# Performance work log

Hardware: AMD Instinct MI355X
Metric: run time of the kernel (lower is better)

Reference implementation:

```python
import jax, jax.numpy as jnp
import numpy as np

S = 1024        # img_size
RADIUS = 512    # number of radial bins
WEIGHT = 1.0


def _bin_idx():
    # Matches torch.meshgrid(arange(-s/2, s/2), ..., indexing='ij') with +0.5 offsets.
    xs = jnp.arange(-S / 2, S / 2, dtype=jnp.float32)
    d = jnp.sqrt((xs[:, None] + 0.5) ** 2 + (xs[None, :] + 0.5) ** 2)  # [S, S]
    # Bin edges are integers 0..RADIUS, so mask (d>=r)&(d<r+1) == (floor(d)==r).
    idx = jnp.floor(d).astype(jnp.int32)
    # Pixels with d >= RADIUS fall in no mask -> overflow bucket RADIUS (dropped later).
    return jnp.where(d < RADIUS, idx, RADIUS).reshape(-1)  # [S*S]


def _power_spec(image):
    ft = jnp.fft.fft2(image)                 # [B, C, S, S] complex
    return jnp.fft.fftshift(jnp.abs(ft) ** 2, axes=(-2, -1))


def _radial_power_spec(ps2d, idx):
    B, C = ps2d.shape[0], ps2d.shape[1]
    flat = ps2d.reshape(B * C, S * S)
    # Histogram reduction: O(S*S) instead of the original O(RADIUS*S*S) dense mask multiply.
    seg = jax.vmap(lambda v: jax.ops.segment_sum(v, idx, num_segments=RADIUS + 1))(flat)
    rad = seg[:, :RADIUS] / (S * S)          # mean over (H, W), drop overflow bucket
    return rad.reshape(B, C, RADIUS).sum(axis=1)  # sum over channel dim


def setup_inputs() -> dict:
    key = jax.random.key(0)
    k1, k2 = jax.random.split(key)
    output = jax.random.normal(k1, (16, 1, S, S), dtype=jnp.float32)
    target = jax.random.normal(k2, (16, 1, S, S), dtype=jnp.float32)
    return {"output": output, "target": target}


def reference(output, target):
    idx = _bin_idx()
    ps_out = _radial_power_spec(_power_spec(output), idx)   # [B, RADIUS]
    ps_tgt = _radial_power_spec(_power_spec(target), idx)   # [B, RADIUS]
    return jnp.mean(jnp.abs(ps_out - ps_tgt)) * WEIGHT
```

## Files before the change

kernel.cpp:

```cpp
#include <hip/hip_runtime.h>
#include <math.h>

#define S 1024
#define RADIUS 512
#define NIMG 32
#define PBX 129

__device__ __forceinline__ float2 cmul(float2 a, float2 b) {
    return make_float2(a.x * b.x - a.y * b.y, a.x * b.y + a.y * b.x);
}
__device__ __forceinline__ float2 cadd(float2 a, float2 b) { return make_float2(a.x + b.x, a.y + b.y); }
__device__ __forceinline__ float2 csub(float2 a, float2 b) { return make_float2(a.x - b.x, a.y - b.y); }

__device__ const float2 C16[8] = {
    {1.0f, 0.0f},
    {0.92387953251128674f, -0.38268343236508978f},
    {0.70710678118654757f, -0.70710678118654746f},
    {0.38268343236508984f, -0.92387953251128674f},
    {0.0f, -1.0f},
    {-0.38268343236508973f, -0.92387953251128674f},
    {-0.70710678118654746f, -0.70710678118654757f},
    {-0.92387953251128663f, -0.38268343236508989f},
};
__device__ const float2 C8T[4] = {
    {1.0f, 0.0f},
    {0.70710678118654757f, -0.70710678118654746f},
    {0.0f, -1.0f},
    {-0.70710678118654746f, -0.70710678118654757f},
};
__device__ const float2 W512T[8] = {
    {1.0f, 0.0f},
    {0.99992470183914454f, -0.012271538285719925f},
    {0.99969881869620425f, -0.024541228522912288f},
    {0.99932238458834954f, -0.036807222941358832f},
    {0.99879545620517241f, -0.049067674327418015f},
    {0.99811811290014918f, -0.061320736302208578f},
    {0.99729045667869021f, -0.073564563599667426f},
    {0.99631261218277800f, -0.085797312344439894f},
};
__device__ const float2 W64T[8] = {
    {1.0f, 0.0f},
    {0.99518472667219693f, -0.098017140329560604f},
    {0.98078528040323044f, -0.19509032201612825f},
    {0.95694033573220886f, -0.29028467725446233f},
    {0.92387953251128674f, -0.38268343236508978f},
    {0.88192126434835505f, -0.47139673682599764f},
    {0.83146961230254524f, -0.55557023301960218f},
    {0.77301045336273699f, -0.63439328416364549f},
};
__device__ const float2 W128P[8] = {
    {1.0f, 0.0f},
    {0.99879545620517241f, -0.049067674327418015f},
    {0.99518472667219693f, -0.098017140329560604f},
    {0.98917650996478101f, -0.14673047445536175f},
    {0.98078528040323044f, -0.19509032201612825f},
    {0.97003125319454397f, -0.24298017990326390f},
    {0.95694033573220886f, -0.29028467725446233f},
    {0.94154406518302081f, -0.33688985339222005f},
};
__device__ const float2 W1024P[8] = {
    {1.0f, 0.0f},
    {0.99998117528260111f, -0.0061358846491544753f},
    {0.99992470183914454f, -0.012271538285719925f},
    {0.99983058179582340f, -0.018406729905804820f},
    {0.99969881869620425f, -0.024541228522912288f},
    {0.99952941750109314f, -0.030674803176636626f},
    {0.99932238458834954f, -0.036807222941358832f},
    {0.99907772775264536f, -0.042938256934940820f},
};

__device__ __forceinline__ void fft16(float2 r[16], float2 T) {
    float2 tc[8];
    #pragma unroll
    for (int u = 0; u < 8; ++u) tc[u] = cmul(T, C16[u]);
    #pragma unroll
    for (int u = 0; u < 8; ++u) {
        float2 a = r[u], b = r[u + 8];
        r[u] = cadd(a, b);
        r[u + 8] = cmul(csub(a, b), tc[u]);
    }
    T = cmul(T, T);
    #pragma unroll
    for (int u = 0; u < 4; ++u) tc[u] = cmul(T, C16[2 * u]);
    #pragma unroll
    for (int g = 0; g < 2; ++g)
        #pragma unroll
        for (int u = 0; u < 4; ++u) {
            int lo = g * 8 + u;
            float2 a = r[lo], b = r[lo + 4];
            r[lo] = cadd(a, b);
            r[lo + 4] = cmul(csub(a, b), tc[u]);
        }
    T = cmul(T, T);
    #pragma unroll
    for (int u = 0; u < 2; ++u) tc[u] = cmul(T, C16[4 * u]);
    #pragma unroll
    for (int g = 0; g < 4; ++g)
        #pragma unroll
        for (int u = 0; u < 2; ++u) {
            int lo = g * 4 + u;
            float2 a = r[lo], b = r[lo + 2];
            r[lo] = cadd(a, b);
            r[lo + 2] = cmul(csub(a, b), tc[u]);
        }
    T = cmul(T, T);
    #pragma unroll
    for (int g = 0; g < 8; ++g) {
        int lo = g * 2;
        float2 a = r[lo], b = r[lo + 1];
        r[lo] = cadd(a, b);
        r[lo + 1] = cmul(csub(a, b), T);
    }
}

__device__ __forceinline__ void fft8(float2 r[8], float2 T) {
    float2 tc[4];
    #pragma unroll
    for (int u = 0; u < 4; ++u) tc[u] = cmul(T, C8T[u]);
    #pragma unroll
    for (int u = 0; u < 4; ++u) {
        float2 a = r[u], b = r[u + 4];
        r[u] = cadd(a, b);
        r[u + 4] = cmul(csub(a, b), tc[u]);
    }
    T = cmul(T, T);
    #pragma unroll
    for (int u = 0; u < 2; ++u) tc[u] = cmul(T, C8T[2 * u]);
    #pragma unroll
    for (int g = 0; g < 2; ++g)
        #pragma unroll
        for (int u = 0; u < 2; ++u) {
            int lo = g * 4 + u;
            float2 a = r[lo], b = r[lo + 2];
            r[lo] = cadd(a, b);
            r[lo + 2] = cmul(csub(a, b), tc[u]);
        }
    T = cmul(T, T);
    #pragma unroll
    for (int g = 0; g < 4; ++g) {
        int lo = g * 2;
        float2 a = r[lo], b = r[lo + 1];
        r[lo] = cadd(a, b);
        r[lo + 1] = cmul(csub(a, b), T);
    }
}

__device__ __forceinline__ void fft_last2(float2 r[16], int c) {
    #pragma unroll
    for (int m = 0; m < 16; ++m) {
        float vx = __shfl_xor(r[m].x, 2, 64);
        float vy = __shfl_xor(r[m].y, 2, 64);
        if (c & 2) {
            float dx = vx - r[m].x, dy = vy - r[m].y;
            if (c & 1) { r[m].x = dy; r[m].y = -dx; }
            else       { r[m].x = dx; r[m].y = dy; }
        } else {
            r[m].x += vx; r[m].y += vy;
        }
    }
    #pragma unroll
    for (int m = 0; m < 16; ++m) {
        float vx = __shfl_xor(r[m].x, 1, 64);
        float vy = __shfl_xor(r[m].y, 1, 64);
        if (c & 1) { r[m].x = vx - r[m].x; r[m].y = vy - r[m].y; }
        else       { r[m].x += vx; r[m].y += vy; }
    }
}

__device__ __forceinline__ int bitrev3(int x) {
    return ((x & 1) << 2) | (x & 2) | ((x >> 2) & 1);
}

__global__ __launch_bounds__(512, 4)
void fft_rows(const float* __restrict__ outp, const float* __restrict__ tgtp,
              float2* __restrict__ WpT, int imgBase) {
    __shared__ float2 buf[4096];
    const int t = threadIdx.x;
    const int w = t >> 6, tau = t & 63;
    const int yy = blockIdx.x * 8 + w;
    const int i = blockIdx.y, g = imgBase + i;
    const float* img = (g < 16 ? outp : tgtp) + (size_t)(g & 15) * S * S;
    const float* r0 = img + (size_t)(2 * yy) * S;
    const float* r1 = r0 + S;

    float2 r[16];
    #pragma unroll
    for (int j = 0; j < 16; ++j) r[j] = make_float2(r0[64 * j + tau], r1[64 * j + tau]);

    fft16(r, cmul(W128P[tau >> 3], W1024P[tau & 7]));

    float2* wb = buf + (w << 9);
    const int b = tau >> 2, c = tau & 3;
    float2 ex[8];
    #pragma unroll
    for (int j = 0; j < 8; ++j) wb[(j << 6) | (tau ^ (j << 2))] = r[j];
    if (b < 8) {
        #pragma unroll
        for (int m = 0; m < 8; ++m)  r[m]      = wb[((b & 7) << 6) + 4 * ((m ^ b) & 15) + c];
        #pragma unroll
        for (int m = 8; m < 16; ++m) ex[m - 8] = wb[((b & 7) << 6) + 4 * ((m ^ b) & 15) + c];
    }
    #pragma unroll
    for (int j = 8; j < 16; ++j) wb[((j & 7) << 6) | (tau ^ (j << 2))] = r[j];
    if (b >= 8) {
        #pragma unroll
        for (int m = 0; m < 8; ++m)  r[m]      = wb[((b & 7) << 6) + 4 * ((m ^ b) & 15) + c];
        #pragma unroll
        for (int m = 8; m < 16; ++m) ex[m - 8] = wb[((b & 7) << 6) + 4 * ((m ^ b) & 15) + c];
    }
    #pragma unroll
    for (int m = 8; m < 16; ++m) r[m] = ex[m - 8];

    fft16(r, W64T[c]);
    fft_last2(r, c);

    const int yy0 = blockIdx.x * 8;
    float2* dst = WpT + (size_t)i * 512 * 1024;
    #pragma unroll
    for (int h = 0; h < 2; ++h) {
        if ((c & 1) == h) {
            #pragma unroll
            for (int m = 0; m < 16; ++m) {
                int n = (b << 6) + 4 * m + c;
                int kh = (int)(__brev((unsigned)n) >> 22) & 511;
                buf[(w << 9) | (kh ^ (w << 1))] = r[m];
            }
        }
        __syncthreads();
        #pragma unroll
        for (int q = 0; q < 8; ++q) {
            int idx = q * 512 + t;
            int uu = idx >> 3, wv = idx & 7;
            float2 val = buf[(wv << 9) | (uu ^ (wv << 1))];
            dst[(size_t)(uu + (h << 9)) * 512 + yy0 + wv] = val;
        }
        __syncthreads();
    }
}

__global__ __launch_bounds__(512, 4)
void fft_cols_bin2(const float2* __restrict__ WpT, float* __restrict__ partial, int imgBase) {
    __shared__ float2 tbuf[8 * 512];
    __shared__ float pref[512];
    __shared__ float cws[8];
    __shared__ float cwx[8];
    const int t = threadIdx.x;
    const int w = t >> 6, tau = t & 63;
    const int i = blockIdx.y, g = imgBase + i;
    const int l = w >> 1;
    const int u = blockIdx.x * 4 + l;
    const int setb = w & 1;
    const bool active = (u <= 512);

    const int b3 = tau >> 3, lam = tau & 7;
    float2 X[8];
    float2* mb = tbuf + (w << 9);

    if (active) {
        const float2* Wimg = WpT + (size_t)i * 512 * 1024;
        const int mu = (1024 - u) & 1023;
        const float2* rowA = Wimg + (size_t)u * 512;
        const float2* rowM = Wimg + (size_t)mu * 512;

        #pragma unroll
        for (int j = 0; j < 8; ++j) {
            float2 A = rowA[64 * j + tau];
            float2 M = rowM[64 * j + tau];
            X[j] = (setb == 0)
                 ? make_float2(0.5f * (A.x + M.x), 0.5f * (A.y - M.y))
                 : make_float2(0.5f * (A.y + M.y), 0.5f * (M.x - A.x));
        }

        fft8(X, cmul(W64T[b3], W512T[lam]));

        #pragma unroll
        for (int j = 0; j < 8; ++j) mb[(j << 6) | (tau ^ (j << 3) ^ j)] = X[j];
        #pragma unroll
        for (int c = 0; c < 8; ++c) X[c] = mb[(b3 << 6) | (((c ^ b3) << 3) | (lam ^ b3))];

        fft8(X, W64T[lam]);

        #pragma unroll
        for (int c = 0; c < 8; ++c) mb[(b3 << 6) | (((c ^ b3) << 3) | (lam ^ b3))] = X[c];
        #pragma unroll
        for (int d = 0; d < 8; ++d) X[d] = mb[(b3 << 6) | (((lam ^ b3) << 3) | (d ^ b3))];

        fft8(X, make_float2(1.0f, 0.0f));

        const int base9 = 8 * bitrev3(lam) + bitrev3(b3);
        #pragma unroll
        for (int d = 0; d < 8; ++d) {
            mb[(bitrev3(d) << 6) + base9] = X[d];
        }
    }
    __syncthreads();

    float p[8];
    if (active) {
        const float2* b0 = tbuf + ((w & ~1) << 9);
        const float2* b1 = tbuf + ((w | 1) << 9);
        const float2 Wtau = cmul(W128P[tau >> 3], W1024P[tau & 7]);
        #pragma unroll
        for (int m = 0; m < 8; ++m) {
            const int f = tau + 64 * m;
            float2 x0 = b0[f];
            float2 x1 = b1[f];
            float2 Wf = cmul(Wtau, C16[m]);
            float2 wx = cmul(Wf, x1);
            float2 G = (setb == 0) ? cadd(x0, wx)
                                   : csub(x0, wx);
            p[m] = G.x * G.x + G.y * G.y;
        }
    }
    __syncthreads();

    float* Prow = (float*)tbuf;
    if (active) {
        #pragma unroll
        for (int m = 0; m < 8; ++m) {
            const int v = tau + 64 * m + (setb << 9);
            Prow[(l << 10) + v] = p[m];
        }
    }
    __syncthreads();

    const int r = t;
    const float r2  = (float)(r * r);
    const float r12 = (float)((r + 1) * (r + 1));
    float acc = 0.0f;

    for (int rowi = 0; rowi < 8; ++rowi) {
        const int ll = rowi >> 1;
        const int mir = rowi & 1;
        const int uu = blockIdx.x * 4 + ll;
        const bool valid = (uu <= 512) && (!mir || (uu >= 1 && uu <= 511));
        float F = 0.0f;
        if (valid) {
            const float* PR = Prow + (ll << 10);
            F = mir ? (PR[t + 1] + PR[(1024 - t) & 1023])
                    : (PR[t] + PR[1023 - t]);
        }
        float s = F;
        #pragma unroll
        for (int off = 1; off < 64; off <<= 1) {
            float n = __shfl_up(s, off, 64);
            if (tau >= off) s += n;
        }
        pref[t] = s;
        if (tau == 63) cws[w] = s;
        __syncthreads();
        if (t < 8) {
            float x = 0.0f;
            #pragma unroll
            for (int j = 0; j < 8; ++j) {
                if (j < t) x += cws[j];
            }
            cwx[t] = x;
        }
        __syncthreads();
        if (valid) {
            const float cuv = mir ? ((float)uu - 0.5f)
                                  : ((uu < 512) ? ((float)uu + 0.5f) : 511.5f);
            const float cu2 = cuv * cuv;
            const float Bv = r12 - cu2;
            if (Bv > 0.0f) {
                const float Av = r2 - cu2;
                float cvlo = (Av > 0.0f) ? sqrtf(Av) : 0.0f;
                float cvhi = sqrtf(Bv);
                int vlo = (int)ceilf(cvlo - 0.5f);
                int vhi = (int)ceilf(cvhi - 0.5f);
                if (vhi > 512) vhi = 512;
                if (vlo < 0) vlo = 0;
                if (vhi > vlo) {
                    float hi = pref[vhi - 1] + cwx[(vhi - 1) >> 6];
                    float lo = (vlo > 0) ? (pref[vlo - 1] + cwx[(vlo - 1) >> 6]) : 0.0f;
                    acc += hi - lo;
                }
            }
        }
        __syncthreads();
    }
    partial[(((size_t)g * PBX) + blockIdx.x) * 512 + t] = acc;
}

__global__ __launch_bounds__(512)
void reduce_partials(const float* __restrict__ partial, float* __restrict__ rad) {
    const int g = blockIdx.x;
    const int t = threadIdx.x;
    const float* p = partial + (size_t)g * PBX * 512;
    float s = 0.0f;
    for (int b = 0; b < PBX; ++b) s += p[(size_t)b * 512 + t];
    rad[(size_t)g * 512 + t] = s;
}

__global__ __launch_bounds__(256)
void final_loss(const float* __restrict__ rad, float* __restrict__ out) {
    __shared__ float red[256];
    const int t = threadIdx.x;
    float acc = 0.0f;
    for (int i = t; i < 16 * RADIUS; i += 256) {
        int bb = i >> 9;
        int rr = i & (RADIUS - 1);
        float o = rad[(size_t)bb * RADIUS + rr];
        float gg = rad[(size_t)(bb + 16) * RADIUS + rr];
        acc += fabsf(o - gg);
    }
    red[t] = acc;
    __syncthreads();
    for (int off = 128; off > 0; off >>= 1) {
        if (t < off) red[t] += red[t + off];
        __syncthreads();
    }
    if (t == 0) {
        out[0] = red[0] / ((float)S * (float)S) / (16.0f * (float)RADIUS);
    }
}

extern "C" void kernel_launch(void* const* d_in, const int* in_sizes, int n_in,
                              void* d_out, int out_size, void* d_ws, size_t ws_size,
                              hipStream_t stream) {
    const float* outp = (const float*)d_in[0];
    const float* tgtp = (const float*)d_in[1];
    float* dout = (float*)d_out;

    char* ws = (char*)d_ws;
    float* rad = (float*)ws;
    const size_t partBytes = (size_t)NIMG * PBX * 512 * sizeof(float);
    float* partial = (float*)(ws + 65536);
    float2* WpT = (float2*)(ws + 65536 + partBytes);
    const size_t perImg = (size_t)512 * 1024 * sizeof(float2);
    size_t used = 65536 + partBytes;
    size_t avail = (ws_size > used) ? (ws_size - used) : 0;
    int chunk = (int)(avail / perImg);
    if (chunk > NIMG) chunk = NIMG;
    if (chunk < 1) chunk = 1;

    for (int base = 0; base < NIMG; base += chunk) {
        int c = (NIMG - base < chunk) ? (NIMG - base) : chunk;
        fft_rows<<<dim3(64, c), 512, 0, stream>>>(outp, tgtp, WpT, base);
        fft_cols_bin2<<<dim3(PBX, c), 512, 0, stream>>>(WpT, partial, base);
    }

    reduce_partials<<<NIMG, 512, 0, stream>>>(partial, rad);
    final_loss<<<1, 256, 0, stream>>>(rad, dout);
}
```

Before: 174.9 us.

## Vectorize row loads/stores and make radial binning wave-local without block barriers

The row FFT now loads input rows with float4 reads staged through shared memory and writes the transposed output with float4 stores instead of scalar float2 accesses. In the column/binning kernel, each wave now owns one (row, mirror) pair and computes its full 512-entry prefix sum with a shuffle carry, so the per-row block-wide barriers and cross-wave scan fixup go away. Each wave then evaluates all 512 radii for its row, and the per-wave bin results are summed across waves through shared memory. This removes many __syncthreads calls at the cost of more per-thread registers (acc[8]) and extra shared-memory traffic.

New measurement: 163.9 us. 1.07x faster.

```diff
diff --git a/kernel.cpp b/kernel.cpp
--- a/kernel.cpp
+++ b/kernel.cpp
@@ -183,13 +183,27 @@
     const float* r0 = img + (size_t)(2 * yy) * S;
     const float* r1 = r0 + S;
 
+    float2* wb = buf + (w << 9);
+    float* wf = (float*)wb;
+
     float2 r[16];
     #pragma unroll
-    for (int j = 0; j < 16; ++j) r[j] = make_float2(r0[64 * j + tau], r1[64 * j + tau]);
+    for (int q = 0; q < 4; ++q) {
+        float4 v = *reinterpret_cast<const float4*>(&r0[q * 256 + 4 * tau]);
+        *reinterpret_cast<float4*>(&wf[q * 256 + 4 * tau]) = v;
+    }
+    #pragma unroll
+    for (int j = 0; j < 16; ++j) r[j].x = wf[64 * j + tau];
+    #pragma unroll
+    for (int q = 0; q < 4; ++q) {
+        float4 v = *reinterpret_cast<const float4*>(&r1[q * 256 + 4 * tau]);
+        *reinterpret_cast<float4*>(&wf[q * 256 + 4 * tau]) = v;
+    }
+    #pragma unroll
+    for (int j = 0; j < 16; ++j) r[j].y = wf[64 * j + tau];
 
     fft16(r, cmul(W128P[tau >> 3], W1024P[tau & 7]));
 
-    float2* wb = buf + (w << 9);
     const int b = tau >> 2, c = tau & 3;
     float2 ex[8];
     #pragma unroll
@@ -228,11 +242,14 @@
         }
         __syncthreads();
         #pragma unroll
-        for (int q = 0; q < 8; ++q) {
-            int idx = q * 512 + t;
-            int uu = idx >> 3, wv = idx & 7;
-            float2 val = buf[(wv << 9) | (uu ^ (wv << 1))];
-            dst[(size_t)(uu + (h << 9)) * 512 + yy0 + wv] = val;
+        for (int q = 0; q < 4; ++q) {
+            int idx4 = q * 512 + t;
+            int p2 = (idx4 & 3) << 1;
+            int uu = idx4 >> 2;
+            float2 v0 = buf[((p2 + 0) << 9) | (uu ^ ((p2 + 0) << 1))];
+            float2 v1 = buf[((p2 + 1) << 9) | (uu ^ ((p2 + 1) << 1))];
+            float4 vv = make_float4(v0.x, v0.y, v1.x, v1.y);
+            *reinterpret_cast<float4*>(&dst[(size_t)(uu + (h << 9)) * 512 + yy0 + p2]) = vv;
         }
         __syncthreads();
     }
@@ -241,9 +258,6 @@
 __global__ __launch_bounds__(512, 4)
 void fft_cols_bin2(const float2* __restrict__ WpT, float* __restrict__ partial, int imgBase) {
     __shared__ float2 tbuf[8 * 512];
-    __shared__ float pref[512];
-    __shared__ float cws[8];
-    __shared__ float cwx[8];
     const int t = threadIdx.x;
     const int w = t >> 6, tau = t & 63;
     const int i = blockIdx.y, g = imgBase + i;
@@ -315,6 +329,7 @@
     __syncthreads();
 
     float* Prow = (float*)tbuf;
+    float* wpref = ((float*)tbuf) + 4096;
     if (active) {
         #pragma unroll
         for (int m = 0; m < 8; ++m) {
@@ -324,21 +339,20 @@
     }
     __syncthreads();
 
-    const int r = t;
-    const float r2  = (float)(r * r);
-    const float r12 = (float)((r + 1) * (r + 1));
-    float acc = 0.0f;
-
-    for (int rowi = 0; rowi < 8; ++rowi) {
-        const int ll = rowi >> 1;
-        const int mir = rowi & 1;
-        const int uu = blockIdx.x * 4 + ll;
-        const bool valid = (uu <= 512) && (!mir || (uu >= 1 && uu <= 511));
+    const int mir = w & 1;
+    const int uu = blockIdx.x * 4 + l;
+    const bool valid = (uu <= 512) && (!mir || (uu >= 1 && uu <= 511));
+    const float* PR = Prow + (l << 10);
+    float* myp = wpref + (w << 9);
+
+    float carry = 0.0f;
+    #pragma unroll
+    for (int k = 0; k < 8; ++k) {
+        const int idx = (k << 6) + tau;
         float F = 0.0f;
         if (valid) {
-            const float* PR = Prow + (ll << 10);
-            F = mir ? (PR[t + 1] + PR[(1024 - t) & 1023])
-                    : (PR[t] + PR[1023 - t]);
+            F = mir ? (PR[idx + 1] + PR[(1024 - idx) & 1023])
+                    : (PR[idx] + PR[1023 - idx]);
         }
         float s = F;
         #pragma unroll
@@ -346,22 +360,20 @@
             float n = __shfl_up(s, off, 64);
             if (tau >= off) s += n;
         }
-        pref[t] = s;
-        if (tau == 63) cws[w] = s;
-        __syncthreads();
-        if (t < 8) {
-            float x = 0.0f;
-            #pragma unroll
-            for (int j = 0; j < 8; ++j) {
-                if (j < t) x += cws[j];
-            }
-            cwx[t] = x;
-        }
-        __syncthreads();
+        myp[idx] = s + carry;
+        carry += __shfl(s, 63, 64);
+    }
+    const float cuv = mir ? ((float)uu - 0.5f)
+                          : ((uu < 512) ? ((float)uu + 0.5f) : 511.5f);
+    const float cu2 = cuv * cuv;
+    float acc[8];
+    #pragma unroll
+    for (int m = 0; m < 8; ++m) {
+        acc[m] = 0.0f;
         if (valid) {
-            const float cuv = mir ? ((float)uu - 0.5f)
-                                  : ((uu < 512) ? ((float)uu + 0.5f) : 511.5f);
-            const float cu2 = cuv * cuv;
+            const int r = tau + (m << 6);
+            const float r2  = (float)(r * r);
+            const float r12 = (float)((r + 1) * (r + 1));
             const float Bv = r12 - cu2;
             if (Bv > 0.0f) {
                 const float Av = r2 - cu2;
@@ -372,15 +384,26 @@
                 if (vhi > 512) vhi = 512;
                 if (vlo < 0) vlo = 0;
                 if (vhi > vlo) {
-                    float hi = pref[vhi - 1] + cwx[(vhi - 1) >> 6];
-                    float lo = (vlo > 0) ? (pref[vlo - 1] + cwx[(vlo - 1) >> 6]) : 0.0f;
-                    acc += hi - lo;
+                    float hi = myp[vhi - 1];
+                    float lo = (vlo > 0) ? myp[vlo - 1] : 0.0f;
+                    acc[m] = hi - lo;
                 }
             }
         }
-        __syncthreads();
-    }
-    partial[(((size_t)g * PBX) + blockIdx.x) * 512 + t] = acc;
+    }
+    __syncthreads();
+
+    float* wavebins = (float*)tbuf;
+    #pragma unroll
+    for (int m = 0; m < 8; ++m) {
+        wavebins[(w << 9) + (m << 6) + tau] = acc[m];
+    }
+    __syncthreads();
+
+    float sum = 0.0f;
+    #pragma unroll
+    for (int ww = 0; ww < 8; ++ww) sum += wavebins[(ww << 9) + t];
+    partial[(((size_t)g * PBX) + blockIdx.x) * 512 + t] = sum;
 }
 
 __global__ __launch_bounds__(512)
```
